# Performance work log

Hardware: AMD Instinct MI355X
Metric: run time of the kernel (lower is better)

The kernel has to match this reference:

```python
import jax, jax.numpy as jnp
import numpy as np

N_NODES = 50000
NUM_FEATURES = 256
HIDDEN_DIM = 64
N_EDGES = 1000000
NEG_SLOPE = 0.2  # PyG GATConv default negative_slope
EPS = 1e-16      # PyG softmax denominator epsilon


def gat_conv(x, src, dst, W, a_src, a_dst, bias, num_nodes):
    """Single-head PyG-style GATConv with self-loops already included in (src, dst).

    x: [N, F_in]; W: [F_in, F_out]; a_src/a_dst: [F_out]; bias: [F_out].
    """
    h = x @ W                                   # [N, F_out]
    alpha_src = h @ a_src                       # [N]
    alpha_dst = h @ a_dst                       # [N]
    e = alpha_src[src] + alpha_dst[dst]         # [E]
    e = jnp.where(e >= 0, e, NEG_SLOPE * e)     # LeakyReLU
    # segment softmax over incoming edges of each destination node
    m = jax.ops.segment_max(e, dst, num_segments=num_nodes)   # [N]
    e = jnp.exp(e - m[dst])                                    # [E]
    s = jax.ops.segment_sum(e, dst, num_segments=num_nodes)   # [N]
    alpha = e / (s[dst] + EPS)                                 # [E]
    out = jax.ops.segment_sum(alpha[:, None] * h[src], dst, num_segments=num_nodes)
    return out + bias


def setup_inputs() -> dict:
    key = jax.random.key(0)
    ks = jax.random.split(key, 12)
    glorot = lambda k, shp: jax.random.normal(k, shp, jnp.float32) * np.sqrt(2.0 / sum(shp))
    return {
        "x": jax.random.normal(ks[0], (N_NODES, NUM_FEATURES), jnp.float32),
        "edge_index": jax.random.randint(ks[1], (2, N_EDGES), 0, N_NODES, jnp.int64),
        "W1": glorot(ks[2], (NUM_FEATURES, HIDDEN_DIM)),
        "a1_src": glorot(ks[3], (HIDDEN_DIM,)),
        "a1_dst": glorot(ks[4], (HIDDEN_DIM,)),
        "b1": jnp.zeros((HIDDEN_DIM,), jnp.float32),
        "W2": glorot(ks[5], (HIDDEN_DIM, HIDDEN_DIM)),
        "a2_src": glorot(ks[6], (HIDDEN_DIM,)),
        "a2_dst": glorot(ks[7], (HIDDEN_DIM,)),
        "b2": jnp.zeros((HIDDEN_DIM,), jnp.float32),
        "fc_w": glorot(ks[8], (2 * HIDDEN_DIM, 1)),
        "fc_b": jnp.zeros((1,), jnp.float32),
    }


def reference(x, edge_index, W1, a1_src, a1_dst, b1, W2, a2_src, a2_dst, b2, fc_w, fc_b):
    num_nodes = x.shape[0]
    src_e, dst_e = edge_index[0], edge_index[1]
    # PyG GATConv adds self-loops by default
    loops = jnp.arange(num_nodes, dtype=edge_index.dtype)
    src = jnp.concatenate([src_e, loops])
    dst = jnp.concatenate([dst_e, loops])

    h = jax.nn.relu(gat_conv(x, src, dst, W1, a1_src, a1_dst, b1, num_nodes))
    h = jax.nn.relu(gat_conv(h, src, dst, W2, a2_src, a2_dst, b2, num_nodes))

    # edge-wise rating prediction on the ORIGINAL edges (no self-loops)
    combined = jnp.concatenate([h[src_e], h[dst_e]], axis=1)  # [E, 2*hidden]
    return combined @ fc_w + fc_b                              # [E, 1]
```

## Files before the change

kernel.cpp:

```cpp
#include <hip/hip_runtime.h>
#include <hip/hip_bf16.h>
#include <hip/hip_fp16.h>

#define NEG_SLOPE 0.2f
#define SEPS 1e-16f
#define CAP 64
#define NB 128
#define BSHIFT 9
#define BCAP 16384
#define CH 4096

using f16x8 = __attribute__((ext_vector_type(8))) _Float16;
using f32x4 = __attribute__((ext_vector_type(4))) float;

__device__ __forceinline__ int edge_at(const void* ei, int is64, long long idx) {
  return is64 ? (int)((const long long*)ei)[idx] : ((const int*)ei)[idx];
}

__global__ void detect_kernel(const unsigned* ei, int* flag) {
  __shared__ int any_nz;
  if (threadIdx.x == 0) any_nz = 0;
  __syncthreads();
  unsigned hi = ei[2 * threadIdx.x + 1];
  if (hi != 0) atomicOr(&any_nz, 1);
  __syncthreads();
  if (threadIdx.x == 0) *flag = (any_nz == 0) ? 1 : 0;
}

__global__ __launch_bounds__(256) void partition_kernel(const void* ei,
                                                        const int* __restrict__ flag,
                                                        int* __restrict__ bcnt,
                                                        unsigned* __restrict__ bdata,
                                                        int E, int N) {
  __shared__ int hist[NB];
  __shared__ int lofs[NB];
  __shared__ int gbase[NB];
  __shared__ unsigned stage[CH];
  __shared__ int gaddr[CH];
  int tid = threadIdx.x;
  long long Etot = (long long)E + N;
  long long base = (long long)blockIdx.x * CH;
  int f = *flag;
  for (int i = tid; i < NB; i += 256) hist[i] = 0;
  __syncthreads();
  unsigned sd[16];
  int lp[16], bk[16];
#pragma unroll
  for (int k = 0; k < 16; ++k) {
    long long i = base + tid + k * 256;
    if (i < Etot) {
      int s = (i < E) ? edge_at(ei, f, i) : (int)(i - E);
      int d = (i < E) ? edge_at(ei, f, (long long)E + i) : (int)(i - E);
      sd[k] = ((unsigned)d << 16) | (unsigned)s;
      bk[k] = d >> BSHIFT;
      lp[k] = atomicAdd(&hist[bk[k]], 1);
    } else {
      bk[k] = -1;
    }
  }
  __syncthreads();
  if (tid < 64) {
    int h0 = hist[2 * tid], h1 = hist[2 * tid + 1];
    int v = h0 + h1, incl = v;
#pragma unroll
    for (int off = 1; off < 64; off <<= 1) {
      int t = __shfl_up(incl, off);
      if (tid >= off) incl += t;
    }
    int excl = incl - v;
    lofs[2 * tid] = excl;
    lofs[2 * tid + 1] = excl + h0;
  }
  if (tid >= 128 && tid < 128 + NB) {
    int b = tid - 128;
    int h = hist[b];
    gbase[b] = h ? atomicAdd(&bcnt[b], h) : 0;
  }
  __syncthreads();
#pragma unroll
  for (int k = 0; k < 16; ++k) {
    if (bk[k] >= 0) {
      int sl = lofs[bk[k]] + lp[k];
      stage[sl] = sd[k];
      gaddr[sl] = bk[k] * BCAP + gbase[bk[k]] + lp[k];
    }
  }
  __syncthreads();
  int cnt_here = (int)((Etot - base < CH) ? (Etot - base) : CH);
  for (int j = tid; j < cnt_here; j += 256) bdata[gaddr[j]] = stage[j];
}

__global__ void build_kernel(const int* __restrict__ bcnt, const unsigned* __restrict__ bdata,
                             int* __restrict__ cnt, unsigned short* __restrict__ csr, int nb) {
  int b = blockIdx.x >> 2, sub = blockIdx.x & 3;
  if (b >= nb) return;
  int n = bcnt[b];
  const unsigned* src = bdata + (size_t)b * BCAP;
  for (int base = sub * 1024; base < n; base += 4096) {
    unsigned v[4];
    int pos[4], d[4];
#pragma unroll
    for (int k = 0; k < 4; ++k) {
      int idx = base + k * 256 + threadIdx.x;
      if (idx < n) {
        v[k] = src[idx];
        d[k] = (int)(v[k] >> 16);
        pos[k] = atomicAdd(&cnt[d[k]], 1);
      } else {
        pos[k] = CAP;
      }
    }
#pragma unroll
    for (int k = 0; k < 4; ++k)
      if (pos[k] < CAP) csr[(size_t)d[k] * CAP + pos[k]] = (unsigned short)(v[k] & 0xFFFFu);
  }
}

template <int K, bool HALF_IN>
__global__ __launch_bounds__(256) void gemm_mfma(const void* __restrict__ Xv,
                                                 const float* __restrict__ W,
                                                 const float* __restrict__ av,
                                                 const float* __restrict__ bv,
                                                 __half* __restrict__ Yh,
                                                 float* __restrict__ oa,
                                                 float* __restrict__ ob, int N) {
  constexpr int PITCH = 40;
  __shared__ __align__(16) char smem[2 * 64 * PITCH * 2];
  _Float16* Al  = (_Float16*)smem;
  _Float16* Btl = Al + 64 * PITCH;
  _Float16* Ep  = (_Float16*)smem;

  int tid = threadIdx.x;
  int wid = tid >> 6, lane = tid & 63;
  int g = lane >> 4, c = lane & 15;
  int row0 = blockIdx.x * 64;
  int sr = tid >> 2, sq = tid & 3;
  int wk = tid >> 4, wq = tid & 15;

  f32x4 acc[4];
#pragma unroll
  for (int n = 0; n < 4; ++n) acc[n] = f32x4{0.f, 0.f, 0.f, 0.f};

  for (int kt = 0; kt < K; kt += 32) {
    {
      int row = row0 + sr;
      f16x8 h = {};
      if (row < N) {
        if (HALF_IN) {
          h = *(const f16x8*)((const _Float16*)Xv + (size_t)row * K + kt + sq * 8);
        } else {
          const float* xp = (const float*)Xv + (size_t)row * K + kt + sq * 8;
          float4 a = *(const float4*)xp;
          float4 b = *(const float4*)(xp + 4);
          h[0] = (_Float16)a.x; h[1] = (_Float16)a.y;
          h[2] = (_Float16)a.z; h[3] = (_Float16)a.w;
          h[4] = (_Float16)b.x; h[5] = (_Float16)b.y;
          h[6] = (_Float16)b.z; h[7] = (_Float16)b.w;
        }
      }
      *(f16x8*)&Al[sr * PITCH + sq * 8] = h;
    }
    {
      float4 w0 = *(const float4*)&W[(size_t)(kt + wk) * 64 + wq * 4];
      float4 w1 = *(const float4*)&W[(size_t)(kt + wk + 16) * 64 + wq * 4];
      Btl[(wq * 4 + 0) * PITCH + wk] = (_Float16)w0.x;
      Btl[(wq * 4 + 1) * PITCH + wk] = (_Float16)w0.y;
      Btl[(wq * 4 + 2) * PITCH + wk] = (_Float16)w0.z;
      Btl[(wq * 4 + 3) * PITCH + wk] = (_Float16)w0.w;
      Btl[(wq * 4 + 0) * PITCH + wk + 16] = (_Float16)w1.x;
      Btl[(wq * 4 + 1) * PITCH + wk + 16] = (_Float16)w1.y;
      Btl[(wq * 4 + 2) * PITCH + wk + 16] = (_Float16)w1.z;
      Btl[(wq * 4 + 3) * PITCH + wk + 16] = (_Float16)w1.w;
    }
    __syncthreads();
    f16x8 af = *(f16x8*)&Al[(wid * 16 + c) * PITCH + g * 8];
#pragma unroll
    for (int n = 0; n < 4; ++n) {
      f16x8 bf = *(f16x8*)&Btl[(n * 16 + c) * PITCH + g * 8];
      acc[n] = __builtin_amdgcn_mfma_f32_16x16x32_f16(af, bf, acc[n], 0, 0, 0);
    }
    __syncthreads();
  }

  {
    float avc[4], bvc[4];
#pragma unroll
    for (int n = 0; n < 4; ++n) { avc[n] = av[n * 16 + c]; bvc[n] = bv[n * 16 + c]; }
#pragma unroll
    for (int r = 0; r < 4; ++r) {
      float pa = 0.f, pb = 0.f;
#pragma unroll
      for (int n = 0; n < 4; ++n) { pa += acc[n][r] * avc[n]; pb += acc[n][r] * bvc[n]; }
#pragma unroll
      for (int off = 1; off < 16; off <<= 1) {
        pa += __shfl_xor(pa, off);
        pb += __shfl_xor(pb, off);
      }
      int row = row0 + wid * 16 + g * 4 + r;
      if (c == 0 && row < N) { oa[row] = pa; ob[row] = pb; }
    }
  }

  __syncthreads();
#pragma unroll
  for (int n = 0; n < 4; ++n)
#pragma unroll
    for (int r = 0; r < 4; ++r)
      Ep[(wid * 16 + g * 4 + r) * 72 + n * 16 + c] = (_Float16)acc[n][r];
  __syncthreads();
  {
    int row = row0 + sr;
    if (row < N) {
      float4 v0 = *(float4*)&Ep[sr * 72 + sq * 8];
      float4 v1 = *(float4*)&Ep[sr * 72 + (sq + 4) * 8];
      ((float4*)(Yh + (size_t)row * 64))[sq] = v0;
      ((float4*)(Yh + (size_t)row * 64))[sq + 4] = v1;
    }
  }
}

__global__ void agg_kernel(const int* __restrict__ cnt, const unsigned short* __restrict__ csr,
                           const __half* __restrict__ H, const float* __restrict__ as_,
                           const float* __restrict__ ad_, const float* __restrict__ bias,
                           __half* __restrict__ out, int N,
                           const float* __restrict__ pw,
                           float* __restrict__ pout, float* __restrict__ qout) {
  int node = (int)((blockIdx.x * blockDim.x + threadIdx.x) >> 6);
  int lane = threadIdx.x & 63;
  if (node >= N) return;
  int deg = cnt[node];
  deg = (deg > CAP) ? CAP : deg;
  const unsigned short* row = csr + (size_t)node * CAP;
  float ad = ad_[node];
  int g = lane >> 3, fl = lane & 7;
  const float4* H16 = (const float4*)H;
  float a[8];
#pragma unroll
  for (int k = 0; k < 8; ++k) a[k] = 0.f;
  float ss = 0.f;

  for (int b = 0; b < deg; b += 32) {
    int idx[4], s[4];
    bool val[4];
    float p[4];
    float4 raw[4];
#pragma unroll
    for (int j = 0; j < 4; ++j) {
      idx[j] = b + j * 8 + g;
      val[j] = idx[j] < deg;
      int ic = idx[j] < CAP - 1 ? idx[j] : CAP - 1;
      s[j] = row[ic];
    }
#pragma unroll
    for (int j = 0; j < 4; ++j) {
      float e = as_[s[j]] + ad;
      e = (e >= 0.f) ? e : NEG_SLOPE * e;
      p[j] = val[j] ? __expf(e) : 0.f;
      raw[j] = H16[(size_t)s[j] * 8 + fl];
    }
#pragma unroll
    for (int j = 0; j < 4; ++j) {
      ss += p[j];
      float2 f0 = __half22float2(*(__half2*)&raw[j].x);
      float2 f1 = __half22float2(*(__half2*)&raw[j].y);
      float2 f2 = __half22float2(*(__half2*)&raw[j].z);
      float2 f3 = __half22float2(*(__half2*)&raw[j].w);
      a[0] += p[j] * f0.x; a[1] += p[j] * f0.y;
      a[2] += p[j] * f1.x; a[3] += p[j] * f1.y;
      a[4] += p[j] * f2.x; a[5] += p[j] * f2.y;
      a[6] += p[j] * f3.x; a[7] += p[j] * f3.y;
    }
  }
#pragma unroll
  for (int off = 8; off <= 32; off <<= 1) {
#pragma unroll
    for (int k = 0; k < 8; ++k) a[k] += __shfl_xor(a[k], off);
    ss += __shfl_xor(ss, off);
  }
  float inv = 1.f / (ss + SEPS);
  float o[8];
#pragma unroll
  for (int k = 0; k < 8; ++k) o[k] = fmaxf(a[k] * inv + bias[8 * fl + k], 0.f);
  if (g == 0) {
    if (out) {
      float4 packed;
      *(__half2*)&packed.x = __floats2half2_rn(o[0], o[1]);
      *(__half2*)&packed.y = __floats2half2_rn(o[2], o[3]);
      *(__half2*)&packed.z = __floats2half2_rn(o[4], o[5]);
      *(__half2*)&packed.w = __floats2half2_rn(o[6], o[7]);
      ((float4*)out)[(size_t)node * 8 + fl] = packed;
    }
    if (pw) {
      float pp = 0.f, qq = 0.f;
#pragma unroll
      for (int k = 0; k < 8; ++k) {
        pp += o[k] * pw[8 * fl + k];
        qq += o[k] * pw[64 + 8 * fl + k];
      }
#pragma unroll
      for (int off = 1; off < 8; off <<= 1) {
        pp += __shfl_xor(pp, off);
        qq += __shfl_xor(qq, off);
      }
      if (fl == 0) { pout[node] = pp; qout[node] = qq; }
    }
  }
}

__global__ void final_kernel(const void* ei, const int* __restrict__ flag,
                             const float* __restrict__ p, const float* __restrict__ q,
                             const float* __restrict__ fcb, float* __restrict__ out,
                             int E, long long T) {
  long long t = (long long)blockIdx.x * blockDim.x + threadIdx.x;
  if (t >= T) return;
  int f = *flag;
  float c = fcb[0];
#pragma unroll
  for (int k = 0; k < 4; ++k) {
    long long i = t + (long long)k * T;
    if (i < E) {
      int s = edge_at(ei, f, i);
      int d = edge_at(ei, f, (long long)E + i);
      out[i] = p[s] + q[d] + c;
    }
  }
}

extern "C" void kernel_launch(void* const* d_in, const int* in_sizes, int n_in,
                              void* d_out, int out_size, void* d_ws, size_t ws_size,
                              hipStream_t stream) {
  const float* x   = (const float*)d_in[0];
  const void*  ei  = d_in[1];
  const float* W1  = (const float*)d_in[2];
  const float* a1s = (const float*)d_in[3];
  const float* a1d = (const float*)d_in[4];
  const float* b1  = (const float*)d_in[5];
  const float* W2  = (const float*)d_in[6];
  const float* a2s = (const float*)d_in[7];
  const float* a2d = (const float*)d_in[8];
  const float* b2  = (const float*)d_in[9];
  const float* fcw = (const float*)d_in[10];
  const float* fcb = (const float*)d_in[11];
  float* out = (float*)d_out;

  int N = in_sizes[0] / 256;
  int E = in_sizes[1] / 2;
  long long Etot = (long long)E + N;
  int nb = (N + ((1 << BSHIFT) - 1)) >> BSHIFT;

  char* w = (char*)d_ws;
  auto alloc = [&](size_t bytes) {
    char* p = w;
    w += (bytes + 255) & ~(size_t)255;
    return p;
  };
  int*            flag    = (int*)alloc(4);
  int*            cnt     = (int*)alloc((size_t)N * 4);
  int*            bcnt    = (int*)alloc((size_t)NB * 4);
  unsigned*       bdata   = (unsigned*)alloc((size_t)NB * BCAP * 4);
  unsigned short* csr     = (unsigned short*)alloc((size_t)N * CAP * 2);
  float*          alpha_s = (float*)alloc((size_t)N * 4);
  float*          alpha_d = (float*)alloc((size_t)N * 4);
  __half*         hA      = (__half*)alloc((size_t)N * 64 * 2);
  __half*         hB      = (__half*)alloc((size_t)N * 64 * 2);
  float*          pbuf    = (float*)alloc((size_t)N * 4);
  float*          qbuf    = (float*)alloc((size_t)N * 4);

  hipMemsetAsync(cnt, 0, ((size_t)N + 256 + NB) * 4, stream);
  detect_kernel<<<1, 256, 0, stream>>>((const unsigned*)ei, flag);
  int pblocks = (int)((Etot + CH - 1) / CH);
  partition_kernel<<<pblocks, 256, 0, stream>>>(ei, flag, bcnt, bdata, E, N);
  build_kernel<<<nb * 4, 256, 0, stream>>>(bcnt, bdata, cnt, csr, nb);

  gemm_mfma<256, false><<<(N + 63) / 64, 256, 0, stream>>>(x, W1, a1s, a1d, hA,
                                                           alpha_s, alpha_d, N);
  agg_kernel<<<(N + 3) / 4, 256, 0, stream>>>(cnt, csr, hA, alpha_s, alpha_d, b1, hB, N,
                                              nullptr, nullptr, nullptr);

  gemm_mfma<64, true><<<(N + 63) / 64, 256, 0, stream>>>(hB, W2, a2s, a2d, hA,
                                                         alpha_s, alpha_d, N);
  agg_kernel<<<(N + 3) / 4, 256, 0, stream>>>(cnt, csr, hA, alpha_s, alpha_d, b2, nullptr, N,
                                              fcw, pbuf, qbuf);

  long long T4 = ((long long)E + 3) / 4;
  final_kernel<<<(int)((T4 + 255) / 256), 256, 0, stream>>>(ei, flag, pbuf, qbuf, fcb, out, E, T4);
}
```

Measured before the change: 152.8 us.

## Fold memset into kernels, prefetch GEMM tiles, unroll aggregation gathers

Three changes. The host memset is removed: the detect kernel now zeroes the bucket counters and the partition kernel zeroes the per-node counts, which saves one launch. The MFMA GEMM loads the next K-tile of A and W into registers before the MFMAs on the current tile, so global latency overlaps compute. The aggregation kernel drops its 32-edge loop and issues all up to 64 neighbour loads (attention scores and features) at once, raising memory-level parallelism at the cost of more registers.

```diff
diff --git a/kernel.cpp b/kernel.cpp
--- a/kernel.cpp
+++ b/kernel.cpp
@@ -17,10 +17,11 @@
   return is64 ? (int)((const long long*)ei)[idx] : ((const int*)ei)[idx];
 }
 
-__global__ void detect_kernel(const unsigned* ei, int* flag) {
+__global__ void detect_kernel(const unsigned* ei, int* flag, int* bcnt) {
   __shared__ int any_nz;
   if (threadIdx.x == 0) any_nz = 0;
   __syncthreads();
+  if (threadIdx.x < NB) bcnt[threadIdx.x] = 0;
   unsigned hi = ei[2 * threadIdx.x + 1];
   if (hi != 0) atomicOr(&any_nz, 1);
   __syncthreads();
@@ -31,6 +32,7 @@
                                                         const int* __restrict__ flag,
                                                         int* __restrict__ bcnt,
                                                         unsigned* __restrict__ bdata,
+                                                        int* __restrict__ cnt,
                                                         int E, int N) {
   __shared__ int hist[NB];
   __shared__ int lofs[NB];
@@ -41,6 +43,7 @@
   long long Etot = (long long)E + N;
   long long base = (long long)blockIdx.x * CH;
   int f = *flag;
+  for (int i = blockIdx.x * 256 + tid; i < N; i += gridDim.x * 256) cnt[i] = 0;
   for (int i = tid; i < NB; i += 256) hist[i] = 0;
   __syncthreads();
   unsigned sd[16];
@@ -136,43 +139,54 @@
   int row0 = blockIdx.x * 64;
   int sr = tid >> 2, sq = tid & 3;
   int wk = tid >> 4, wq = tid & 15;
+  bool arow_ok = (row0 + sr) < N;
+  const char* aptr = HALF_IN ? (const char*)((const _Float16*)Xv + (size_t)(row0 + sr) * K + sq * 8)
+                             : (const char*)((const float*)Xv + (size_t)(row0 + sr) * K + sq * 8);
 
   f32x4 acc[4];
 #pragma unroll
   for (int n = 0; n < 4; ++n) acc[n] = f32x4{0.f, 0.f, 0.f, 0.f};
 
+  auto loadA = [&](int kt) -> f16x8 {
+    f16x8 h = {};
+    if (arow_ok) {
+      if (HALF_IN) {
+        h = *(const f16x8*)(aptr + (size_t)kt * 2);
+      } else {
+        const float* xp = (const float*)(aptr + (size_t)kt * 4);
+        float4 a = *(const float4*)xp;
+        float4 b = *(const float4*)(xp + 4);
+        h[0] = (_Float16)a.x; h[1] = (_Float16)a.y;
+        h[2] = (_Float16)a.z; h[3] = (_Float16)a.w;
+        h[4] = (_Float16)b.x; h[5] = (_Float16)b.y;
+        h[6] = (_Float16)b.z; h[7] = (_Float16)b.w;
+      }
+    }
+    return h;
+  };
+
+  f16x8 ha = loadA(0);
+  float4 w0 = *(const float4*)&W[(size_t)wk * 64 + wq * 4];
+  float4 w1 = *(const float4*)&W[(size_t)(wk + 16) * 64 + wq * 4];
+
   for (int kt = 0; kt < K; kt += 32) {
-    {
-      int row = row0 + sr;
-      f16x8 h = {};
-      if (row < N) {
-        if (HALF_IN) {
-          h = *(const f16x8*)((const _Float16*)Xv + (size_t)row * K + kt + sq * 8);
-        } else {
-          const float* xp = (const float*)Xv + (size_t)row * K + kt + sq * 8;
-          float4 a = *(const float4*)xp;
-          float4 b = *(const float4*)(xp + 4);
-          h[0] = (_Float16)a.x; h[1] = (_Float16)a.y;
-          h[2] = (_Float16)a.z; h[3] = (_Float16)a.w;
-          h[4] = (_Float16)b.x; h[5] = (_Float16)b.y;
-          h[6] = (_Float16)b.z; h[7] = (_Float16)b.w;
-        }
-      }
-      *(f16x8*)&Al[sr * PITCH + sq * 8] = h;
-    }
-    {
-      float4 w0 = *(const float4*)&W[(size_t)(kt + wk) * 64 + wq * 4];
-      float4 w1 = *(const float4*)&W[(size_t)(kt + wk + 16) * 64 + wq * 4];
-      Btl[(wq * 4 + 0) * PITCH + wk] = (_Float16)w0.x;
-      Btl[(wq * 4 + 1) * PITCH + wk] = (_Float16)w0.y;
-      Btl[(wq * 4 + 2) * PITCH + wk] = (_Float16)w0.z;
-      Btl[(wq * 4 + 3) * PITCH + wk] = (_Float16)w0.w;
-      Btl[(wq * 4 + 0) * PITCH + wk + 16] = (_Float16)w1.x;
-      Btl[(wq * 4 + 1) * PITCH + wk + 16] = (_Float16)w1.y;
-      Btl[(wq * 4 + 2) * PITCH + wk + 16] = (_Float16)w1.z;
-      Btl[(wq * 4 + 3) * PITCH + wk + 16] = (_Float16)w1.w;
-    }
+    *(f16x8*)&Al[sr * PITCH + sq * 8] = ha;
+    Btl[(wq * 4 + 0) * PITCH + wk] = (_Float16)w0.x;
+    Btl[(wq * 4 + 1) * PITCH + wk] = (_Float16)w0.y;
+    Btl[(wq * 4 + 2) * PITCH + wk] = (_Float16)w0.z;
+    Btl[(wq * 4 + 3) * PITCH + wk] = (_Float16)w0.w;
+    Btl[(wq * 4 + 0) * PITCH + wk + 16] = (_Float16)w1.x;
+    Btl[(wq * 4 + 1) * PITCH + wk + 16] = (_Float16)w1.y;
+    Btl[(wq * 4 + 2) * PITCH + wk + 16] = (_Float16)w1.z;
+    Btl[(wq * 4 + 3) * PITCH + wk + 16] = (_Float16)w1.w;
     __syncthreads();
+    f16x8 ha_n = {};
+    float4 w0_n, w1_n;
+    if (kt + 32 < K) {
+      ha_n = loadA(kt + 32);
+      w0_n = *(const float4*)&W[(size_t)(kt + 32 + wk) * 64 + wq * 4];
+      w1_n = *(const float4*)&W[(size_t)(kt + 32 + wk + 16) * 64 + wq * 4];
+    }
     f16x8 af = *(f16x8*)&Al[(wid * 16 + c) * PITCH + g * 8];
 #pragma unroll
     for (int n = 0; n < 4; ++n) {
@@ -180,6 +194,7 @@
       acc[n] = __builtin_amdgcn_mfma_f32_16x16x32_f16(af, bf, acc[n], 0, 0, 0);
     }
     __syncthreads();
+    ha = ha_n; w0 = w0_n; w1 = w1_n;
   }
 
   {
@@ -233,42 +248,40 @@
   const unsigned short* row = csr + (size_t)node * CAP;
   float ad = ad_[node];
   int g = lane >> 3, fl = lane & 7;
+  int nj = (deg > g) ? ((deg - g + 7) >> 3) : 0;
   const float4* H16 = (const float4*)H;
+
+  int sv[8];
+#pragma unroll
+  for (int j = 0; j < 8; ++j) sv[j] = row[j * 8 + g];
+  float ev[8];
+  float4 raw[8];
+#pragma unroll
+  for (int j = 0; j < 8; ++j)
+    if (j < nj) ev[j] = as_[sv[j]];
+#pragma unroll
+  for (int j = 0; j < 8; ++j)
+    if (j < nj) raw[j] = H16[(size_t)sv[j] * 8 + fl];
+
   float a[8];
 #pragma unroll
   for (int k = 0; k < 8; ++k) a[k] = 0.f;
   float ss = 0.f;
-
-  for (int b = 0; b < deg; b += 32) {
-    int idx[4], s[4];
-    bool val[4];
-    float p[4];
-    float4 raw[4];
-#pragma unroll
-    for (int j = 0; j < 4; ++j) {
-      idx[j] = b + j * 8 + g;
-      val[j] = idx[j] < deg;
-      int ic = idx[j] < CAP - 1 ? idx[j] : CAP - 1;
-      s[j] = row[ic];
-    }
-#pragma unroll
-    for (int j = 0; j < 4; ++j) {
-      float e = as_[s[j]] + ad;
+#pragma unroll
+  for (int j = 0; j < 8; ++j) {
+    if (j < nj) {
+      float e = ev[j] + ad;
       e = (e >= 0.f) ? e : NEG_SLOPE * e;
-      p[j] = val[j] ? __expf(e) : 0.f;
-      raw[j] = H16[(size_t)s[j] * 8 + fl];
-    }
-#pragma unroll
-    for (int j = 0; j < 4; ++j) {
-      ss += p[j];
+      float p = __expf(e);
+      ss += p;
       float2 f0 = __half22float2(*(__half2*)&raw[j].x);
       float2 f1 = __half22float2(*(__half2*)&raw[j].y);
       float2 f2 = __half22float2(*(__half2*)&raw[j].z);
       float2 f3 = __half22float2(*(__half2*)&raw[j].w);
-      a[0] += p[j] * f0.x; a[1] += p[j] * f0.y;
-      a[2] += p[j] * f1.x; a[3] += p[j] * f1.y;
-      a[4] += p[j] * f2.x; a[5] += p[j] * f2.y;
-      a[6] += p[j] * f3.x; a[7] += p[j] * f3.y;
+      a[0] += p * f0.x; a[1] += p * f0.y;
+      a[2] += p * f1.x; a[3] += p * f1.y;
+      a[4] += p * f2.x; a[5] += p * f2.y;
+      a[6] += p * f3.x; a[7] += p * f3.y;
     }
   }
 #pragma unroll
@@ -366,10 +379,9 @@
   float*          pbuf    = (float*)alloc((size_t)N * 4);
   float*          qbuf    = (float*)alloc((size_t)N * 4);
 
-  hipMemsetAsync(cnt, 0, ((size_t)N + 256 + NB) * 4, stream);
-  detect_kernel<<<1, 256, 0, stream>>>((const unsigned*)ei, flag);
+  detect_kernel<<<1, 256, 0, stream>>>((const unsigned*)ei, flag, bcnt);
   int pblocks = (int)((Etot + CH - 1) / CH);
-  partition_kernel<<<pblocks, 256, 0, stream>>>(ei, flag, bcnt, bdata, E, N);
+  partition_kernel<<<pblocks, 256, 0, stream>>>(ei, flag, bcnt, bdata, cnt, E, N);
   build_kernel<<<nb * 4, 256, 0, stream>>>(bcnt, bdata, cnt, csr, nb);
 
   gemm_mfma<256, false><<<(N + 63) / 64, 256, 0, stream>>>(x, W1, a1s, a1d, hA,
```

Result: faster. 137.7 us (-9.9%).
